# Kernel tuning notes

Measured on AMD Instinct MI355X. Metric: run time of the kernel, lower is better.

## Reference

```python
import jax, jax.numpy as jnp
import numpy as np

N = 50000
E = 1600000
IN_F = 256
OUT_F = 128
ALPHA = 0.2  # LeakyReLU negative slope


def setup_inputs() -> dict:
    key = jax.random.key(0)
    k1, k2, k3, k4, k5, k6 = jax.random.split(key, 6)
    h = jax.random.normal(k1, (N, IN_F), dtype=jnp.float32)
    src = jax.random.randint(k2, (E,), 0, N, dtype=jnp.int64)
    dst = jax.random.randint(k3, (E,), 0, N, dtype=jnp.int64)
    # xavier_uniform-style init
    def xavier(k, shape):
        bound = np.sqrt(6.0 / (shape[0] + shape[1]))
        return jax.random.uniform(k, shape, jnp.float32, -bound, bound)
    W = xavier(k4, (IN_F, OUT_F))
    a_src = xavier(k5, (OUT_F, 1))
    a_dst = xavier(k6, (OUT_F, 1))
    return {"h": h, "src": src, "dst": dst, "W": W, "a_src": a_src, "a_dst": a_dst}


def reference(h, src, dst, W, a_src, a_dst):
    n = h.shape[0]
    Wh = h @ W                                  # [N, OUT_F] dense GEMM
    f1 = (Wh @ a_src)[:, 0]                     # [N]
    f2 = (Wh @ a_dst)[:, 0]                     # [N]
    e = f1[src] + f2[dst]                       # [E] edge-wise gather
    e = jnp.where(e > 0, e, ALPHA * e)          # LeakyReLU
    # sparse softmax over each row (segment = src/row index)
    m = jax.ops.segment_max(e, src, num_segments=n)
    ex = jnp.exp(e - m[src])
    denom = jax.ops.segment_sum(ex, src, num_segments=n)
    att = ex / denom[src]                       # [E] normalized attention
    # sparse-dense matmul: h_prime[i] = sum_j att[ij] * Wh[j]
    h_prime = jax.ops.segment_sum(att[:, None] * Wh[dst], src, num_segments=n)
    return jax.nn.elu(h_prime)
```

## Files before the change

### kernel.cpp

```cpp
#include <hip/hip_runtime.h>
#include <hip/hip_bf16.h>
#include <math.h>

#define IN_F 256
#define OUT_F 128
#define ALPHA 0.2f

#define BSH 7
#define BNODES 128
#define CHUNK 8192
#define NBK 512
#define CAP 5120

typedef __attribute__((ext_vector_type(8))) short short8;
typedef __attribute__((ext_vector_type(4))) float f32x4;
typedef __attribute__((ext_vector_type(2))) float f32x2;

static __device__ __forceinline__ unsigned short f2bf(float x) {
    union { __hip_bfloat16 h; unsigned short u; } cv;
    cv.h = __float2bfloat16(x);
    return cv.u;
}

static __device__ __forceinline__ f32x2 up2(unsigned int u) {
    union { float f; unsigned int i; } lo, hi;
    lo.i = u << 16;
    hi.i = u & 0xFFFF0000u;
    return (f32x2){lo.f, hi.f};
}

__global__ __launch_bounds__(512) void scatter_gemm_kernel(
        const int* __restrict__ src, const int* __restrict__ dst,
        int* __restrict__ cursor, unsigned int* __restrict__ bin, int e, int nb,
        const float* __restrict__ h, const float* __restrict__ W,
        const float* __restrict__ a_src, const float* __restrict__ a_dst,
        unsigned short* __restrict__ WhbQ, float* __restrict__ f1,
        float* __restrict__ f2, int n, int nsc) {
    __shared__ union {
        struct {
            unsigned int ebuf[CHUNK];
            int lh[NBK];
            int ebase[NBK];
            int lx[NBK];
            int gbase[NBK];
            int wsum[8];
        } sc;
        struct {
            unsigned short a[128 * 40];
            unsigned short b[128 * 40];
        } ge;
    } sm;
    int tid = threadIdx.x;

    if ((int)blockIdx.x < nsc) {
        int base = blockIdx.x * CHUNK;
        int count = e - base; if (count > CHUNK) count = CHUNK;

        for (int i = tid; i < nb; i += 512) sm.sc.lh[i] = 0;
        __syncthreads();
        for (int i = tid; i < count; i += 512) atomicAdd(&sm.sc.lh[src[base + i] >> BSH], 1);
        __syncthreads();
        int v = (tid < nb) ? sm.sc.lh[tid] : 0;
        int lane = tid & 63, wvv = tid >> 6;
        int s = v;
#pragma unroll
        for (int off = 1; off < 64; off <<= 1) {
            int t = __shfl_up(s, off, 64);
            if (lane >= off) s += t;
        }
        if (lane == 63) sm.sc.wsum[wvv] = s;
        __syncthreads();
        if (tid < 8) {
            int ws = sm.sc.wsum[tid];
#pragma unroll
            for (int off = 1; off < 8; off <<= 1) {
                int t = __shfl_up(ws, off, 64);
                if (tid >= off) ws += t;
            }
            sm.sc.wsum[tid] = ws;
        }
        __syncthreads();
        int ex = s + (wvv ? sm.sc.wsum[wvv - 1] : 0) - v;
        if (tid < nb) {
            sm.sc.ebase[tid] = ex;
            sm.sc.lx[tid] = ex;
        }
        __syncthreads();
        for (int i = tid; i < count; i += 512) {
            int sv = src[base + i], d = dst[base + i];
            int b = sv >> BSH;
            int p = atomicAdd(&sm.sc.lx[b], 1);
            sm.sc.ebuf[p] = ((unsigned int)(sv & (BNODES - 1)) << 17) | (unsigned int)d;
        }
        __syncthreads();
        if (tid < nb) {
            int c = sm.sc.lh[tid];
            sm.sc.gbase[tid] = c ? atomicAdd(&cursor[tid], c) : 0;
        }
        __syncthreads();
        int wave = tid >> 6, lane2 = tid & 63;
        for (int b = wave; b < nb; b += 8) {
            int c = sm.sc.lh[b], eb = sm.sc.ebase[b], gb = sm.sc.gbase[b];
            size_t gb0 = (size_t)b * CAP + gb;
            for (int l = lane2; l < c; l += 64) bin[gb0 + l] = sm.sc.ebuf[eb + l];
        }
    } else {
        int bid = blockIdx.x - nsc;
        int wv = tid >> 6, lane = tid & 63;
        int m = lane & 15, quad = lane >> 4;
        int r0 = bid * 128;

        f32x4 acc[8];
#pragma unroll
        for (int c = 0; c < 8; c++) acc[c] = (f32x4){0.f, 0.f, 0.f, 0.f};

        int bcol = tid & 127;
        int bkq  = tid >> 7;

        for (int k0 = 0; k0 < IN_F; k0 += 32) {
            {
                int arow = tid >> 3;
                int kq = tid & 7;
#pragma unroll
                for (int p = 0; p < 2; p++) {
                    int row = arow + p * 64;
                    int grow = r0 + row;
                    float4 v = make_float4(0.f, 0.f, 0.f, 0.f);
                    if (grow < n) v = *(const float4*)&h[(size_t)grow * IN_F + k0 + kq * 4];
                    ushort4 b;
                    b.x = f2bf(v.x); b.y = f2bf(v.y); b.z = f2bf(v.z); b.w = f2bf(v.w);
                    *(ushort4*)&sm.ge.a[row * 40 + kq * 4] = b;
                }
            }
            {
                float vw[8];
#pragma unroll
                for (int j = 0; j < 8; ++j)
                    vw[j] = W[(size_t)(k0 + bkq * 8 + j) * OUT_F + bcol];
                union { short8 v; unsigned short u[8]; } pk;
#pragma unroll
                for (int j = 0; j < 8; ++j) pk.u[j] = f2bf(vw[j]);
                *(short8*)&sm.ge.b[bcol * 40 + bkq * 8] = pk.v;
            }
            __syncthreads();
            short8 af = *(const short8*)&sm.ge.a[(wv * 16 + m) * 40 + quad * 8];
#pragma unroll
            for (int c = 0; c < 8; c++) {
                short8 bfv = *(const short8*)&sm.ge.b[(c * 16 + m) * 40 + quad * 8];
                acc[c] = __builtin_amdgcn_mfma_f32_16x16x32_bf16(af, bfv, acc[c], 0, 0, 0);
            }
            __syncthreads();
        }

        int base_row = r0 + wv * 16 + quad * 4;
#pragma unroll
        for (int reg = 0; reg < 4; reg++) {
            int rg = base_row + reg;
            if (rg < n) {
#pragma unroll
                for (int c = 0; c < 8; c++) {
                    WhbQ[(size_t)(c >> 1) * n * 32 + (size_t)rg * 32 + (c & 1) * 16 + m] =
                        f2bf(acc[c][reg]);
                }
            }
        }

        float a1[8], a2[8];
#pragma unroll
        for (int c = 0; c < 8; c++) {
            a1[c] = a_src[c * 16 + m];
            a2[c] = a_dst[c * 16 + m];
        }
        float p1[4] = {0.f, 0.f, 0.f, 0.f}, p2[4] = {0.f, 0.f, 0.f, 0.f};
#pragma unroll
        for (int c = 0; c < 8; c++)
#pragma unroll
            for (int reg = 0; reg < 4; reg++) {
                p1[reg] += acc[c][reg] * a1[c];
                p2[reg] += acc[c][reg] * a2[c];
            }
#pragma unroll
        for (int mask = 1; mask < 16; mask <<= 1)
#pragma unroll
            for (int reg = 0; reg < 4; reg++) {
                p1[reg] += __shfl_xor(p1[reg], mask, 64);
                p2[reg] += __shfl_xor(p2[reg], mask, 64);
            }
        if (m == 0) {
#pragma unroll
            for (int reg = 0; reg < 4; reg++) {
                int rg = base_row + reg;
                if (rg < n) { f1[rg] = p1[reg]; f2[rg] = p2[reg]; }
            }
        }
    }
}

__global__ __launch_bounds__(512) void sort_kernel(
        const int* __restrict__ cursor, const unsigned int* __restrict__ bin,
        const float* __restrict__ f1, const float* __restrict__ f2,
        unsigned int* __restrict__ edatp, int* __restrict__ offs,
        int* __restrict__ deg, float* __restrict__ inv, int n) {
    __shared__ unsigned int eP[CAP];
    __shared__ int lh[BNODES];
    __shared__ int st[BNODES];
    __shared__ int cur[BNODES];
    __shared__ int scn[BNODES];
    __shared__ float lf1[BNODES];
    __shared__ float lden[BNODES];
    int b = blockIdx.x;
    int tid = threadIdx.x;
    int base = b * CAP;
    int K = cursor[b];
    if (K > CAP) K = CAP;

    if (tid < BNODES) {
        lh[tid] = 0;
        lden[tid] = 0.f;
        int node = (b << BSH) + tid;
        lf1[tid] = (node < n) ? f1[node] : 0.f;
    }
    __syncthreads();

    unsigned int pe[10];
#pragma unroll
    for (int u = 0; u < 10; ++u) {
        int i = tid + u * 512;
        if (i < K) {
            unsigned int p = bin[base + i];
            pe[u] = p;
            atomicAdd(&lh[p >> 17], 1);
        }
    }
    __syncthreads();

    if (tid < BNODES) {
        int lane = tid & 63;
        int s = lh[tid];
#pragma unroll
        for (int off = 1; off < 64; off <<= 1) {
            int t = __shfl_up(s, off, 64);
            if (lane >= off) s += t;
        }
        scn[tid] = s;
    }
    __syncthreads();
    if (tid < BNODES) {
        int incl = scn[tid] + ((tid >= 64) ? scn[63] : 0);
        int start = incl - lh[tid];
        st[tid] = start;
        cur[tid] = start;
    }
    __syncthreads();

#pragma unroll
    for (int u = 0; u < 10; ++u) {
        int i = tid + u * 512;
        if (i < K) {
            unsigned int p = pe[u];
            int ls_ = p >> 17;
            int d = p & 0x1FFFF;
            int r = atomicAdd(&cur[ls_], 1);
            float e = lf1[ls_] + f2[d];
            e = e > 0.f ? e : ALPHA * e;
            float ex = __expf(e);
            atomicAdd(&lden[ls_], ex);
            eP[r] = ((unsigned int)d << 16) | (unsigned int)f2bf(ex);
        }
    }
    __syncthreads();

    if (tid < BNODES) {
        int node = (b << BSH) + tid;
        if (node < n) {
            offs[node] = base + st[tid];
            deg[node] = lh[tid];
            inv[node] = lh[tid] ? 1.f / lden[tid] : 0.f;
        }
    }
    for (int i = tid; i < K; i += 512) edatp[base + i] = eP[i];
}

__global__ __launch_bounds__(256) void aggp_kernel(
        const unsigned int* __restrict__ edatp, const int* __restrict__ offs,
        const int* __restrict__ deg, const float* __restrict__ inv,
        const unsigned int* __restrict__ WhbQ, float* __restrict__ out, int n) {
    int b = blockIdx.x >> 2;
    int q = blockIdx.x & 3;
    int tid = threadIdx.x;
    int wv = tid >> 6, lane = tid & 63;
    int c4 = lane & 3;
    int e2 = (lane >> 2) & 1;
    int slot = lane >> 3;
    unsigned int nm1 = (unsigned int)(n - 1);
    const unsigned int* wq = WhbQ + (size_t)q * n * 16 + (c4 << 2);

    for (int gi = 0; gi < 4; ++gi) {
        int node = (b << BSH) + (wv << 5) + (gi << 3) + slot;
        bool valid = node < n;
        int dg = valid ? deg[node] : 0;
        int off = valid ? offs[node] : 0;
        int jend = off + dg;
        int T = (dg + 1) >> 1;
#pragma unroll
        for (int mask = 8; mask < 64; mask <<= 1) {
            int o = __shfl_xor(T, mask, 64);
            T = o > T ? o : T;
        }
        f32x2 a0 = {0.f, 0.f}, a1 = {0.f, 0.f}, a2 = {0.f, 0.f}, a3 = {0.f, 0.f};
        if (T) {
            int j = off + e2;
            unsigned int ec0 = edatp[j < jend ? j : off];
            int j1 = j + 2;
            unsigned int ec1 = edatp[j1 < jend ? j1 : off];
            unsigned int r0 = ec0 >> 16;
            uint4 w0 = *(const uint4*)&wq[(size_t)(r0 < nm1 ? r0 : nm1) << 4];
            for (int t = 0; t < T; ++t) {
                int j2 = j1 + 2;
                unsigned int ec2 = edatp[j2 < jend ? j2 : off];
                unsigned int r1 = ec1 >> 16;
                uint4 w1 = *(const uint4*)&wq[(size_t)(r1 < nm1 ? r1 : nm1) << 4];
                union { float f; unsigned int u; } xb;
                xb.u = (ec0 & 0xFFFFu) << 16;
                float x = (j < jend) ? xb.f : 0.f;
                f32x2 xx = {x, x};
                a0 += xx * up2(w0.x); a1 += xx * up2(w0.y);
                a2 += xx * up2(w0.z); a3 += xx * up2(w0.w);
                j = j1; j1 = j2; ec0 = ec1; ec1 = ec2; w0 = w1;
            }
        }
        a0.x += __shfl_xor(a0.x, 4, 64); a0.y += __shfl_xor(a0.y, 4, 64);
        a1.x += __shfl_xor(a1.x, 4, 64); a1.y += __shfl_xor(a1.y, 4, 64);
        a2.x += __shfl_xor(a2.x, 4, 64); a2.y += __shfl_xor(a2.y, 4, 64);
        a3.x += __shfl_xor(a3.x, 4, 64); a3.y += __shfl_xor(a3.y, 4, 64);
        if (e2 == 0 && valid) {
            float iv = inv[node];
            float r[8];
            r[0] = a0.x * iv; r[1] = a0.y * iv; r[2] = a1.x * iv; r[3] = a1.y * iv;
            r[4] = a2.x * iv; r[5] = a2.y * iv; r[6] = a3.x * iv; r[7] = a3.y * iv;
#pragma unroll
            for (int k = 0; k < 8; ++k) r[k] = r[k] > 0.f ? r[k] : __expf(r[k]) - 1.f;
            float* op = &out[(size_t)node * OUT_F + (q << 5) + (c4 << 3)];
            *(float4*)&op[0] = make_float4(r[0], r[1], r[2], r[3]);
            *(float4*)&op[4] = make_float4(r[4], r[5], r[6], r[7]);
        }
    }
}

extern "C" void kernel_launch(void* const* d_in, const int* in_sizes, int n_in,
                              void* d_out, int out_size, void* d_ws, size_t ws_size,
                              hipStream_t stream) {
    const float* h     = (const float*)d_in[0];
    const int*   src   = (const int*)d_in[1];
    const int*   dst   = (const int*)d_in[2];
    const float* W     = (const float*)d_in[3];
    const float* a_src = (const float*)d_in[4];
    const float* a_dst = (const float*)d_in[5];
    float* out = (float*)d_out;

    const int N = in_sizes[0] / IN_F;
    const int E = in_sizes[1];
    const int NB = (N + BNODES - 1) >> BSH;
    const int NCH = (E + CHUNK - 1) / CHUNK;
    const int GB = (N + 127) / 128;

    char* ws = (char*)d_ws;
    size_t off = 0;
    auto alloc = [&](size_t bytes) -> void* {
        void* p = ws + off;
        off += (bytes + 255) & ~(size_t)255;
        return p;
    };
    unsigned short* WhbQ = (unsigned short*)alloc((size_t)N * OUT_F * 2);
    float* f1     = (float*)alloc((size_t)N * 4);
    float* f2     = (float*)alloc((size_t)N * 4);
    int*   cursor = (int*)alloc((size_t)NB * 4);
    int*   offs   = (int*)alloc((size_t)N * 4);
    int*   deg    = (int*)alloc((size_t)N * 4);
    float* inv    = (float*)alloc((size_t)N * 4);
    unsigned int* bin   = (unsigned int*)alloc((size_t)NB * CAP * 4);
    unsigned int* edatp = (unsigned int*)alloc((size_t)NB * CAP * 4);
    (void)ws_size; (void)n_in; (void)out_size;

    hipMemsetAsync(cursor, 0, (size_t)NB * 4, stream);
    scatter_gemm_kernel<<<NCH + GB, 512, 0, stream>>>(src, dst, cursor, bin, E, NB,
                                                      h, W, a_src, a_dst, WhbQ, f1, f2, N, NCH);
    sort_kernel<<<NB, 512, 0, stream>>>(cursor, bin, f1, f2, edatp, offs, deg, inv, N);
    aggp_kernel<<<NB * 4, 256, 0, stream>>>(edatp, offs, deg, inv,
                                            (const unsigned int*)WhbQ, out, N);
}
```

Before: 216.7 us.

## Pad per-node edge lists to multiples of four and vectorize aggregation loads

The sort kernel now pads each node's edge segment to a multiple of four entries, so the aggregation kernel can read four packed edges at once with a single uint4 load. Each node is handled by 4 lanes instead of 8, with a four-deep gather of Wh rows per iteration. The grid is doubled so each block covers half of a node bucket. Padding costs extra bin capacity (writes are clamped at CAP), and the padding slots are left uninitialized, relying on the dg mask to zero them.

```diff
diff --git a/kernel.cpp b/kernel.cpp
--- a/kernel.cpp
+++ b/kernel.cpp
@@ -27,6 +27,12 @@
     lo.i = u << 16;
     hi.i = u & 0xFFFF0000u;
     return (f32x2){lo.f, hi.f};
+}
+
+static __device__ __forceinline__ float bfw(unsigned int ec, bool v) {
+    union { float f; unsigned int u; } xb;
+    xb.u = (ec & 0xFFFFu) << 16;
+    return v ? xb.f : 0.f;
 }
 
 __global__ __launch_bounds__(512) void scatter_gemm_kernel(
@@ -208,6 +214,7 @@
     __shared__ int scn[BNODES];
     __shared__ float lf1[BNODES];
     __shared__ float lden[BNODES];
+    __shared__ int kpadS;
     int b = blockIdx.x;
     int tid = threadIdx.x;
     int base = b * CAP;
@@ -236,7 +243,7 @@
 
     if (tid < BNODES) {
         int lane = tid & 63;
-        int s = lh[tid];
+        int s = (lh[tid] + 3) & ~3;
 #pragma unroll
         for (int off = 1; off < 64; off <<= 1) {
             int t = __shfl_up(s, off, 64);
@@ -246,10 +253,12 @@
     }
     __syncthreads();
     if (tid < BNODES) {
+        int pdg = (lh[tid] + 3) & ~3;
         int incl = scn[tid] + ((tid >= 64) ? scn[63] : 0);
-        int start = incl - lh[tid];
+        int start = incl - pdg;
         st[tid] = start;
         cur[tid] = start;
+        if (tid == BNODES - 1) kpadS = incl;
     }
     __syncthreads();
 
@@ -265,7 +274,7 @@
             e = e > 0.f ? e : ALPHA * e;
             float ex = __expf(e);
             atomicAdd(&lden[ls_], ex);
-            eP[r] = ((unsigned int)d << 16) | (unsigned int)f2bf(ex);
+            if (r < CAP) eP[r] = ((unsigned int)d << 16) | (unsigned int)f2bf(ex);
         }
     }
     __syncthreads();
@@ -278,72 +287,94 @@
             inv[node] = lh[tid] ? 1.f / lden[tid] : 0.f;
         }
     }
-    for (int i = tid; i < K; i += 512) edatp[base + i] = eP[i];
+    int Kpad = kpadS < CAP ? kpadS : CAP;
+    for (int i = tid; i < Kpad; i += 512) edatp[base + i] = eP[i];
 }
 
 __global__ __launch_bounds__(256) void aggp_kernel(
         const unsigned int* __restrict__ edatp, const int* __restrict__ offs,
         const int* __restrict__ deg, const float* __restrict__ inv,
         const unsigned int* __restrict__ WhbQ, float* __restrict__ out, int n) {
-    int b = blockIdx.x >> 2;
     int q = blockIdx.x & 3;
+    int idx = blockIdx.x >> 2;
+    int b = idx >> 1, half = idx & 1;
     int tid = threadIdx.x;
     int wv = tid >> 6, lane = tid & 63;
+    int slot = lane >> 2;
     int c4 = lane & 3;
-    int e2 = (lane >> 2) & 1;
-    int slot = lane >> 3;
     unsigned int nm1 = (unsigned int)(n - 1);
     const unsigned int* wq = WhbQ + (size_t)q * n * 16 + (c4 << 2);
-
-    for (int gi = 0; gi < 4; ++gi) {
-        int node = (b << BSH) + (wv << 5) + (gi << 3) + slot;
-        bool valid = node < n;
-        int dg = valid ? deg[node] : 0;
-        int off = valid ? offs[node] : 0;
-        int jend = off + dg;
-        int T = (dg + 1) >> 1;
-#pragma unroll
-        for (int mask = 8; mask < 64; mask <<= 1) {
-            int o = __shfl_xor(T, mask, 64);
-            T = o > T ? o : T;
-        }
-        f32x2 a0 = {0.f, 0.f}, a1 = {0.f, 0.f}, a2 = {0.f, 0.f}, a3 = {0.f, 0.f};
-        if (T) {
-            int j = off + e2;
-            unsigned int ec0 = edatp[j < jend ? j : off];
-            int j1 = j + 2;
-            unsigned int ec1 = edatp[j1 < jend ? j1 : off];
-            unsigned int r0 = ec0 >> 16;
-            uint4 w0 = *(const uint4*)&wq[(size_t)(r0 < nm1 ? r0 : nm1) << 4];
-            for (int t = 0; t < T; ++t) {
-                int j2 = j1 + 2;
-                unsigned int ec2 = edatp[j2 < jend ? j2 : off];
-                unsigned int r1 = ec1 >> 16;
-                uint4 w1 = *(const uint4*)&wq[(size_t)(r1 < nm1 ? r1 : nm1) << 4];
-                union { float f; unsigned int u; } xb;
-                xb.u = (ec0 & 0xFFFFu) << 16;
-                float x = (j < jend) ? xb.f : 0.f;
-                f32x2 xx = {x, x};
-                a0 += xx * up2(w0.x); a1 += xx * up2(w0.y);
-                a2 += xx * up2(w0.z); a3 += xx * up2(w0.w);
-                j = j1; j1 = j2; ec0 = ec1; ec1 = ec2; w0 = w1;
-            }
-        }
-        a0.x += __shfl_xor(a0.x, 4, 64); a0.y += __shfl_xor(a0.y, 4, 64);
-        a1.x += __shfl_xor(a1.x, 4, 64); a1.y += __shfl_xor(a1.y, 4, 64);
-        a2.x += __shfl_xor(a2.x, 4, 64); a2.y += __shfl_xor(a2.y, 4, 64);
-        a3.x += __shfl_xor(a3.x, 4, 64); a3.y += __shfl_xor(a3.y, 4, 64);
-        if (e2 == 0 && valid) {
-            float iv = inv[node];
-            float r[8];
-            r[0] = a0.x * iv; r[1] = a0.y * iv; r[2] = a1.x * iv; r[3] = a1.y * iv;
-            r[4] = a2.x * iv; r[5] = a2.y * iv; r[6] = a3.x * iv; r[7] = a3.y * iv;
-#pragma unroll
-            for (int k = 0; k < 8; ++k) r[k] = r[k] > 0.f ? r[k] : __expf(r[k]) - 1.f;
-            float* op = &out[(size_t)node * OUT_F + (q << 5) + (c4 << 3)];
-            *(float4*)&op[0] = make_float4(r[0], r[1], r[2], r[3]);
-            *(float4*)&op[4] = make_float4(r[4], r[5], r[6], r[7]);
-        }
+    int node = (b << BSH) + (half << 6) + (wv << 4) + slot;
+    bool valid = node < n;
+    int dg = valid ? deg[node] : 0;
+    int off = valid ? offs[node] : b * CAP;
+    int bend = b * CAP + CAP;
+    if (off > bend - 4) off = bend - 4;
+    int myC = (dg + 3) >> 2;
+    int mc2 = (bend - off) >> 2;
+    if (myC > mc2) myC = mc2;
+    int T = myC;
+#pragma unroll
+    for (int mask = 4; mask < 64; mask <<= 1) {
+        int o = __shfl_xor(T, mask, 64);
+        T = o > T ? o : T;
+    }
+    f32x2 a0 = {0.f, 0.f}, a1 = {0.f, 0.f}, a2 = {0.f, 0.f}, a3 = {0.f, 0.f};
+    if (T) {
+        const uint4* ed4 = (const uint4*)edatp + (off >> 2);
+        int lastC = myC > 0 ? myC - 1 : 0;
+        uint4 curc = ed4[0];
+        uint4 nxt = ed4[1 < myC ? 1 : lastC];
+        unsigned int rr;
+        uint4 W0, W1, W2, W3;
+        rr = curc.x >> 16; if (rr > nm1) rr = nm1; W0 = *(const uint4*)&wq[(size_t)rr << 4];
+        rr = curc.y >> 16; if (rr > nm1) rr = nm1; W1 = *(const uint4*)&wq[(size_t)rr << 4];
+        rr = curc.z >> 16; if (rr > nm1) rr = nm1; W2 = *(const uint4*)&wq[(size_t)rr << 4];
+        rr = curc.w >> 16; if (rr > nm1) rr = nm1; W3 = *(const uint4*)&wq[(size_t)rr << 4];
+        float x0 = bfw(curc.x, 0 < dg), x1 = bfw(curc.y, 1 < dg);
+        float x2 = bfw(curc.z, 2 < dg), x3 = bfw(curc.w, 3 < dg);
+        for (int t = 1; t < T; ++t) {
+            uint4 fut = ed4[t + 1 < myC ? t + 1 : lastC];
+            uint4 N0, N1, N2, N3;
+            rr = nxt.x >> 16; if (rr > nm1) rr = nm1; N0 = *(const uint4*)&wq[(size_t)rr << 4];
+            rr = nxt.y >> 16; if (rr > nm1) rr = nm1; N1 = *(const uint4*)&wq[(size_t)rr << 4];
+            rr = nxt.z >> 16; if (rr > nm1) rr = nm1; N2 = *(const uint4*)&wq[(size_t)rr << 4];
+            rr = nxt.w >> 16; if (rr > nm1) rr = nm1; N3 = *(const uint4*)&wq[(size_t)rr << 4];
+            f32x2 xx;
+            xx = (f32x2){x0, x0};
+            a0 += xx * up2(W0.x); a1 += xx * up2(W0.y); a2 += xx * up2(W0.z); a3 += xx * up2(W0.w);
+            xx = (f32x2){x1, x1};
+            a0 += xx * up2(W1.x); a1 += xx * up2(W1.y); a2 += xx * up2(W1.z); a3 += xx * up2(W1.w);
+            xx = (f32x2){x2, x2};
+            a0 += xx * up2(W2.x); a1 += xx * up2(W2.y); a2 += xx * up2(W2.z); a3 += xx * up2(W2.w);
+            xx = (f32x2){x3, x3};
+            a0 += xx * up2(W3.x); a1 += xx * up2(W3.y); a2 += xx * up2(W3.z); a3 += xx * up2(W3.w);
+            int b4 = t << 2;
+            x0 = bfw(nxt.x, b4 + 0 < dg); x1 = bfw(nxt.y, b4 + 1 < dg);
+            x2 = bfw(nxt.z, b4 + 2 < dg); x3 = bfw(nxt.w, b4 + 3 < dg);
+            W0 = N0; W1 = N1; W2 = N2; W3 = N3;
+            nxt = fut;
+        }
+        f32x2 xx;
+        xx = (f32x2){x0, x0};
+        a0 += xx * up2(W0.x); a1 += xx * up2(W0.y); a2 += xx * up2(W0.z); a3 += xx * up2(W0.w);
+        xx = (f32x2){x1, x1};
+        a0 += xx * up2(W1.x); a1 += xx * up2(W1.y); a2 += xx * up2(W1.z); a3 += xx * up2(W1.w);
+        xx = (f32x2){x2, x2};
+        a0 += xx * up2(W2.x); a1 += xx * up2(W2.y); a2 += xx * up2(W2.z); a3 += xx * up2(W2.w);
+        xx = (f32x2){x3, x3};
+        a0 += xx * up2(W3.x); a1 += xx * up2(W3.y); a2 += xx * up2(W3.z); a3 += xx * up2(W3.w);
+    }
+    if (valid) {
+        float iv = inv[node];
+        float r[8];
+        r[0] = a0.x * iv; r[1] = a0.y * iv; r[2] = a1.x * iv; r[3] = a1.y * iv;
+        r[4] = a2.x * iv; r[5] = a2.y * iv; r[6] = a3.x * iv; r[7] = a3.y * iv;
+#pragma unroll
+        for (int k = 0; k < 8; ++k) r[k] = r[k] > 0.f ? r[k] : __expf(r[k]) - 1.f;
+        float* op = &out[(size_t)node * OUT_F + (q << 5) + (c4 << 3)];
+        *(float4*)&op[0] = make_float4(r[0], r[1], r[2], r[3]);
+        *(float4*)&op[4] = make_float4(r[4], r[5], r[6], r[7]);
     }
 }
 
@@ -386,6 +417,6 @@
     scatter_gemm_kernel<<<NCH + GB, 512, 0, stream>>>(src, dst, cursor, bin, E, NB,
                                                       h, W, a_src, a_dst, WhbQ, f1, f2, N, NCH);
     sort_kernel<<<NB, 512, 0, stream>>>(cursor, bin, f1, f2, edatp, offs, deg, inv, N);
-    aggp_kernel<<<NB * 4, 256, 0, stream>>>(edatp, offs, deg, inv,
+    aggp_kernel<<<NB * 8, 256, 0, stream>>>(edatp, offs, deg, inv,
                                             (const unsigned int*)WhbQ, out, N);
 }
```

Measured after the change: 208.7 us. 3.7% less time.
